# Kernel tuning notes

Hardware: AMD Instinct MI355X
Metric: run time of the kernel (lower is better)

The kernel has to match this reference:

```python
import jax, jax.numpy as jnp
import numpy as np

B, MAXLEN = 256, 10000
N_ATOMS, N_BONDS, N_ANG, N_TOR = 2000, 1999, 1998, 1997
NBT, NAT, NTT = 50, 100, 200
EPS = 1e-8


def setup_inputs() -> dict:
    rng = np.random.default_rng(0)
    feats = np.zeros((B, MAXLEN, 9), np.float32)
    # col 0: atom types
    feats[:, :N_ATOMS, 0] = rng.integers(0, 20, (B, N_ATOMS))
    # col 5: flattened coords [3*N]
    coords = (rng.standard_normal((B, N_ATOMS, 3)) * 2.0).astype(np.float32)
    feats[:, :3 * N_ATOMS, 5] = coords.reshape(B, -1)
    # col 6: bonds (i, j, type) along a chain
    i = np.arange(N_BONDS, dtype=np.float32)
    bonds = np.zeros((B, N_BONDS, 3), np.float32)
    bonds[..., 0] = i; bonds[..., 1] = i + 1
    bonds[..., 2] = rng.integers(0, NBT, (B, N_BONDS))
    feats[:, :3 * N_BONDS, 6] = bonds.reshape(B, -1)
    # col 7: angles (i, j, k, type)
    a = np.arange(N_ANG, dtype=np.float32)
    angs = np.zeros((B, N_ANG, 4), np.float32)
    angs[..., 0] = a; angs[..., 1] = a + 1; angs[..., 2] = a + 2
    angs[..., 3] = rng.integers(0, NAT, (B, N_ANG))
    feats[:, :4 * N_ANG, 7] = angs.reshape(B, -1)
    # col 8: torsions (i, j, k, l, type)
    t = np.arange(N_TOR, dtype=np.float32)
    tors = np.zeros((B, N_TOR, 5), np.float32)
    tors[..., 0] = t; tors[..., 1] = t + 1; tors[..., 2] = t + 2; tors[..., 3] = t + 3
    tors[..., 4] = rng.integers(0, NTT, (B, N_TOR))
    feats[:, :5 * N_TOR, 8] = tors.reshape(B, -1)
    # per-column valid lengths
    lengths = np.zeros((B, 9), np.int32)
    lengths[:, 0] = N_ATOMS
    lengths[:, 5] = 3 * N_ATOMS
    lengths[:, 6] = 3 * N_BONDS
    lengths[:, 7] = 4 * N_ANG
    lengths[:, 8] = 5 * N_TOR
    # learned params: (k, eq_value, multiplicity) per type row
    P = NBT + NAT + NTT
    opt = np.abs(rng.standard_normal((P, 3))).astype(np.float32)
    opt[:, 2] = rng.integers(1, 4, P).astype(np.float32)
    return {
        "features": jnp.asarray(feats),
        "lengths": jnp.asarray(lengths),
        "opt_pars": jnp.asarray(opt),
        "bond_type": jnp.arange(NBT, dtype=jnp.float32),
        "angle_type": jnp.arange(NAT, dtype=jnp.float32) + NBT,
        "tor_type": jnp.arange(NTT, dtype=jnp.float32) + NBT + NAT,
    }


def _gather(coords, idx):
    # coords [B,N,3], idx [B,M] -> [B,M,3]
    return jnp.take_along_axis(
        coords, jnp.broadcast_to(idx[..., None], idx.shape + (3,)), axis=1)


def _energy(features, lengths, opt_pars, bond_map, angle_map, tor_map):
    Bn = features.shape[0]
    coords = features[:, :3 * N_ATOMS, 5].reshape(Bn, N_ATOMS, 3)
    bonds = features[:, :3 * N_BONDS, 6].reshape(Bn, N_BONDS, 3).astype(jnp.int32)
    angs = features[:, :4 * N_ANG, 7].reshape(Bn, N_ANG, 4).astype(jnp.int32)
    tors = features[:, :5 * N_TOR, 8].reshape(Bn, N_TOR, 5).astype(jnp.int32)

    # ---- bonds: harmonic E = k * (r - r0)^2 ----
    ri, rj = _gather(coords, bonds[..., 0]), _gather(coords, bonds[..., 1])
    r = jnp.sqrt(jnp.sum((ri - rj) ** 2, -1) + EPS)          # [B,NB]
    pb = opt_pars[bond_map[bonds[..., 2]]]                   # [B,NB,3]
    eb = pb[..., 0] * (r - pb[..., 1]) ** 2
    mb = jnp.arange(N_BONDS)[None, :] < (lengths[:, 6:7] // 3)
    ebonds = jnp.sum(jnp.where(mb, eb, 0.0), -1)

    # ---- angles: harmonic E = k * (theta - theta0)^2 ----
    ai, aj, ak = (_gather(coords, angs[..., c]) for c in range(3))
    u, v = ai - aj, ak - aj
    cos = jnp.sum(u * v, -1) * jax.lax.rsqrt(
        (jnp.sum(u * u, -1) + EPS) * (jnp.sum(v * v, -1) + EPS))
    theta = jnp.arccos(jnp.clip(cos, -1.0 + 1e-6, 1.0 - 1e-6))
    pa = opt_pars[angle_map[angs[..., 3]]]
    ea = pa[..., 0] * (theta - pa[..., 1]) ** 2
    ma = jnp.arange(N_ANG)[None, :] < (lengths[:, 7:8] // 4)
    eangles = jnp.sum(jnp.where(ma, ea, 0.0), -1)

    # ---- torsions: E = k * (1 + cos(n*phi - phi0)) ----
    ti, tj, tk, tl = (_gather(coords, tors[..., c]) for c in range(4))
    b1, b2, b3 = tj - ti, tk - tj, tl - tk
    n1 = jnp.cross(b1, b2)
    n2 = jnp.cross(b2, b3)
    b2h = b2 * jax.lax.rsqrt(jnp.sum(b2 * b2, -1, keepdims=True) + EPS)
    m1 = jnp.cross(n1, b2h)
    phi = jnp.arctan2(jnp.sum(m1 * n2, -1), jnp.sum(n1 * n2, -1))
    pt = opt_pars[tor_map[tors[..., 4]]]
    et = pt[..., 0] * (1.0 + jnp.cos(pt[..., 2] * phi - pt[..., 1]))
    mt = jnp.arange(N_TOR)[None, :] < (lengths[:, 8:9] // 5)
    etors = jnp.sum(jnp.where(mt, et, 0.0), -1)

    return ebonds + eangles + etors                          # [B]


def reference(features, lengths, opt_pars, bond_type, angle_type, tor_type):
    return _energy(features, lengths, opt_pars,
                   bond_type.astype(jnp.int32),
                   angle_type.astype(jnp.int32),
                   tor_type.astype(jnp.int32))
```

## Files before the change

### kernel.cpp

```cpp
#include <hip/hip_runtime.h>
#include <math.h>


#define EBS 1024

constexpr int MAXLEN = 10000;
constexpr int NBT = 50, NAT = 100, NTT = 200;
constexpr float EPS = 1e-8f;

constexpr int OFF_SC  = 0;
constexpr int OFF_SB  = OFF_SC  + 6000 * 4;
constexpr int OFF_SA  = OFF_SB  + 2000 * 8;
constexpr int OFF_ST  = OFF_SA  + 2000 * 8;
constexpr int OFF_SBP = OFF_ST  + 2000 * 16;
constexpr int OFF_SAP = OFF_SBP + NBT * 2 * 4;
constexpr int OFF_STP = OFF_SAP + NAT * 2 * 4;
constexpr int OFF_SW  = OFF_STP + NTT * 4 * 4;
constexpr int SMEM_BYTES = OFF_SW + 16 * 4;

__device__ __forceinline__ float acos_fast(float x) {
    float t = fabsf(x);
    float p = fmaf(t, -0.0187293f, 0.0742610f);
    p = fmaf(p, t, -0.2121144f);
    p = fmaf(p, t, 1.5707288f);
    float r = sqrtf(1.0f - t) * p;
    return (x >= 0.0f) ? r : (3.14159265358979f - r);
}

__global__ __launch_bounds__(EBS) void energy_kernel(
    const float* __restrict__ features,
    const int*   __restrict__ lengths,
    const float* __restrict__ opt_pars,
    const float* __restrict__ bond_type,
    const float* __restrict__ angle_type,
    const float* __restrict__ tor_type,
    float*       __restrict__ out)
{
    extern __shared__ __align__(16) char smem[];
    float*          sc  = (float*)(smem + OFF_SC);
    ushort4*        sb4 = (ushort4*)(smem + OFF_SB);
    ushort4*        sa4 = (ushort4*)(smem + OFF_SA);
    unsigned short* st  = (unsigned short*)(smem + OFF_ST);
    ushort4*        st4 = (ushort4*)(smem + OFF_ST);
    float*          sbp = (float*)(smem + OFF_SBP);
    float*          sap = (float*)(smem + OFF_SAP);
    float*          stp = (float*)(smem + OFF_STP);
    float*          sw  = (float*)(smem + OFF_SW);
    unsigned short* sbf = (unsigned short*)(smem + OFF_SB);
    unsigned short* saf = (unsigned short*)(smem + OFF_SA);

    const int b   = blockIdx.x;
    const int tid = threadIdx.x;
    const float* __restrict__ fb = features + (size_t)b * MAXLEN * 9;

    for (int i = tid; i < NBT; i += EBS) {
        int idx = (int)bond_type[i];
        sbp[2*i+0] = opt_pars[3*idx+0];
        sbp[2*i+1] = opt_pars[3*idx+1];
    }
    for (int i = tid; i < NAT; i += EBS) {
        int idx = (int)angle_type[i];
        sap[2*i+0] = opt_pars[3*idx+0];
        sap[2*i+1] = opt_pars[3*idx+1];
    }
    for (int i = tid; i < NTT; i += EBS) {
        int idx = (int)tor_type[i];
        float k  = opt_pars[3*idx+0];
        float p0 = opt_pars[3*idx+1];
        float n  = opt_pars[3*idx+2];
        stp[4*i+0] = k;
        stp[4*i+1] = cosf(p0);
        stp[4*i+2] = sinf(p0);
        stp[4*i+3] = n;
    }

    #pragma unroll 2
    for (int i = tid; i < MAXLEN; i += EBS) {
        const float* __restrict__ row = fb + 9 * i + 5;
        float vc = row[0];
        float vb = row[1];
        float va = row[2];
        float vt = row[3];
        if (i < 6000) {
            sc[i] = vc;
            int t = i / 3, slot = i - 3 * t;
            if (i < 5997) sbf[4 * t + slot] = (unsigned short)(int)vb;
        }
        if (i < 7992) saf[i] = (unsigned short)(int)va;
        if (i < 9985) {
            int t = i / 5, slot = i - 5 * t;
            st[8 * t + slot] = (unsigned short)(int)vt;
        }
    }
    __syncthreads();

    float acc = 0.0f;

    {
        const int nb = lengths[b * 9 + 6] / 3;
        for (int t = tid; t < nb; t += EBS) {
            ushort4 q = sb4[t];
            int i = q.x, j = q.y, ty = q.z;
            float dx = sc[3*i+0] - sc[3*j+0];
            float dy = sc[3*i+1] - sc[3*j+1];
            float dz = sc[3*i+2] - sc[3*j+2];
            float r  = sqrtf(dx*dx + dy*dy + dz*dz + EPS);
            float d  = r - sbp[2*ty+1];
            acc += sbp[2*ty+0] * d * d;
        }
    }

    {
        const int na = lengths[b * 9 + 7] / 4;
        for (int t = tid; t < na; t += EBS) {
            ushort4 q = sa4[t];
            int i = q.x, j = q.y, k_ = q.z, ty = q.w;
            float jx = sc[3*j+0], jy = sc[3*j+1], jz = sc[3*j+2];
            float ux = sc[3*i+0] - jx, uy = sc[3*i+1] - jy, uz = sc[3*i+2] - jz;
            float vx = sc[3*k_+0] - jx, vy = sc[3*k_+1] - jy, vz = sc[3*k_+2] - jz;
            float uv = ux*vx + uy*vy + uz*vz;
            float uu = ux*ux + uy*uy + uz*uz;
            float vv = vx*vx + vy*vy + vz*vz;
            float cth = uv * rsqrtf((uu + EPS) * (vv + EPS));
            cth = fminf(fmaxf(cth, -1.0f + 1e-6f), 1.0f - 1e-6f);
            float theta = acos_fast(cth);
            float d = theta - sap[2*ty+1];
            acc += sap[2*ty+0] * d * d;
        }
    }

    {
        const int nt = lengths[b * 9 + 8] / 5;
        for (int t = tid; t < nt; t += EBS) {
            ushort4 q = st4[2*t];
            int ty = st[8*t+4];
            int i = q.x, j = q.y, k_ = q.z, l = q.w;
            float ix = sc[3*i+0],  iy = sc[3*i+1],  iz = sc[3*i+2];
            float jx = sc[3*j+0],  jy = sc[3*j+1],  jz = sc[3*j+2];
            float kx = sc[3*k_+0], ky = sc[3*k_+1], kz = sc[3*k_+2];
            float lx = sc[3*l+0],  ly = sc[3*l+1],  lz = sc[3*l+2];
            float b1x = jx - ix, b1y = jy - iy, b1z = jz - iz;
            float b2x = kx - jx, b2y = ky - jy, b2z = kz - jz;
            float b3x = lx - kx, b3y = ly - ky, b3z = lz - kz;
            float n1x = b1y*b2z - b1z*b2y;
            float n1y = b1z*b2x - b1x*b2z;
            float n1z = b1x*b2y - b1y*b2x;
            float n2x = b2y*b3z - b2z*b3y;
            float n2y = b2z*b3x - b2x*b3z;
            float n2z = b2x*b3y - b2y*b3x;
            float inv = rsqrtf(b2x*b2x + b2y*b2y + b2z*b2z + EPS);
            float hx = b2x * inv, hy = b2y * inv, hz = b2z * inv;
            float m1x = n1y*hz - n1z*hy;
            float m1y = n1z*hx - n1x*hz;
            float m1z = n1x*hy - n1y*hx;
            float sy = m1x*n2x + m1y*n2y + m1z*n2z;
            float sx = n1x*n2x + n1y*n2y + n1z*n2z;
            float rinv = rsqrtf(sx*sx + sy*sy + 1e-30f);
            float c1 = sx * rinv, s1 = sy * rinv;
            float c2 = fmaf(2.0f*c1, c1, -1.0f);
            float s2 = 2.0f * s1 * c1;
            float c3 = fmaf(2.0f*c1, c2, -c1);
            float s3 = fmaf(2.0f*c1, s2, -s1);
            float k  = stp[4*ty+0];
            float cp = stp[4*ty+1];
            float sp = stp[4*ty+2];
            int   ni = (int)stp[4*ty+3];
            float cn = (ni == 1) ? c1 : ((ni == 2) ? c2 : c3);
            float sn = (ni == 1) ? s1 : ((ni == 2) ? s2 : s3);
            acc += k * (1.0f + cn * cp + sn * sp);
        }
    }

    for (int off = 32; off > 0; off >>= 1)
        acc += __shfl_down(acc, off, 64);
    const int wave = tid >> 6, lane = tid & 63;
    if (lane == 0) sw[wave] = acc;
    __syncthreads();
    if (tid == 0) {
        float v = 0.0f;
        #pragma unroll
        for (int w = 0; w < EBS / 64; ++w) v += sw[w];
        out[b] = v;
    }
}

extern "C" void kernel_launch(void* const* d_in, const int* in_sizes, int n_in,
                              void* d_out, int out_size, void* d_ws, size_t ws_size,
                              hipStream_t stream) {
    const float* features   = (const float*)d_in[0];
    const int*   lengths    = (const int*)  d_in[1];
    const float* opt_pars   = (const float*)d_in[2];
    const float* bond_type  = (const float*)d_in[3];
    const float* angle_type = (const float*)d_in[4];
    const float* tor_type   = (const float*)d_in[5];
    float* out = (float*)d_out;

    hipFuncSetAttribute((const void*)energy_kernel,
                        hipFuncAttributeMaxDynamicSharedMemorySize, SMEM_BYTES);

    const int B = out_size;
    energy_kernel<<<B, EBS, SMEM_BYTES, stream>>>(
        features, lengths, opt_pars, bond_type, angle_type, tor_type, out);
}
```

Measured before the change: 148.2 us.

## Split fused energy kernel into compact, per-term energy, and reduce kernels

Replaces the single block-per-molecule kernel, which staged everything in shared memory, with four launches. A prep kernel builds the parameter tables, a grid-wide compact kernel writes coordinates and index quads to workspace, and the energy kernel uses 24 chunks per molecule with one thread per bond, angle or torsion. A final kernel reduces the partial sums. The goal is more parallelism and better occupancy than 256 blocks of 1024 threads with large shared-memory use, at the cost of extra launches, global-memory round trips through the workspace, and uncoalesced coordinate gathers from global memory.

```diff
diff --git a/kernel.cpp b/kernel.cpp
--- a/kernel.cpp
+++ b/kernel.cpp
@@ -2,21 +2,20 @@
 #include <math.h>
 
 
-#define EBS 1024
-
+constexpr int BATCH  = 256;
 constexpr int MAXLEN = 10000;
 constexpr int NBT = 50, NAT = 100, NTT = 200;
 constexpr float EPS = 1e-8f;
-
-constexpr int OFF_SC  = 0;
-constexpr int OFF_SB  = OFF_SC  + 6000 * 4;
-constexpr int OFF_SA  = OFF_SB  + 2000 * 8;
-constexpr int OFF_ST  = OFF_SA  + 2000 * 8;
-constexpr int OFF_SBP = OFF_ST  + 2000 * 16;
-constexpr int OFF_SAP = OFF_SBP + NBT * 2 * 4;
-constexpr int OFF_STP = OFF_SAP + NAT * 2 * 4;
-constexpr int OFF_SW  = OFF_STP + NTT * 4 * 4;
-constexpr int SMEM_BYTES = OFF_SW + 16 * 4;
+constexpr int NCH = 24;
+
+constexpr size_t OFF_RBP = 0;
+constexpr size_t OFF_RAP = OFF_RBP + NBT * 2 * 4;
+constexpr size_t OFF_RTP = OFF_RAP + NAT * 2 * 4;
+constexpr size_t OFF_CC  = OFF_RTP + NTT * 4 * 4;
+constexpr size_t OFF_BQ  = OFF_CC  + (size_t)BATCH * 6000 * 4;
+constexpr size_t OFF_AQ  = OFF_BQ  + (size_t)BATCH * 8192 * 2;
+constexpr size_t OFF_TQ  = OFF_AQ  + (size_t)BATCH * 8192 * 2;
+constexpr size_t OFF_PT  = OFF_TQ  + (size_t)BATCH * 16384 * 2;
 
 __device__ __forceinline__ float acos_fast(float x) {
     float t = fabsf(x);
@@ -27,118 +26,122 @@
     return (x >= 0.0f) ? r : (3.14159265358979f - r);
 }
 
-__global__ __launch_bounds__(EBS) void energy_kernel(
-    const float* __restrict__ features,
-    const int*   __restrict__ lengths,
+__global__ __launch_bounds__(256) void prep_kernel(
     const float* __restrict__ opt_pars,
     const float* __restrict__ bond_type,
     const float* __restrict__ angle_type,
     const float* __restrict__ tor_type,
-    float*       __restrict__ out)
-{
-    extern __shared__ __align__(16) char smem[];
-    float*          sc  = (float*)(smem + OFF_SC);
-    ushort4*        sb4 = (ushort4*)(smem + OFF_SB);
-    ushort4*        sa4 = (ushort4*)(smem + OFF_SA);
-    unsigned short* st  = (unsigned short*)(smem + OFF_ST);
-    ushort4*        st4 = (ushort4*)(smem + OFF_ST);
-    float*          sbp = (float*)(smem + OFF_SBP);
-    float*          sap = (float*)(smem + OFF_SAP);
-    float*          stp = (float*)(smem + OFF_STP);
-    float*          sw  = (float*)(smem + OFF_SW);
-    unsigned short* sbf = (unsigned short*)(smem + OFF_SB);
-    unsigned short* saf = (unsigned short*)(smem + OFF_SA);
-
-    const int b   = blockIdx.x;
+    float* __restrict__ rbp, float* __restrict__ rap, float* __restrict__ rtp)
+{
+    const int i = threadIdx.x;
+    if (i < NBT) {
+        int idx = (int)bond_type[i];
+        rbp[2*i+0] = opt_pars[3*idx+0];
+        rbp[2*i+1] = opt_pars[3*idx+1];
+    }
+    if (i < NAT) {
+        int idx = (int)angle_type[i];
+        rap[2*i+0] = opt_pars[3*idx+0];
+        rap[2*i+1] = opt_pars[3*idx+1];
+    }
+    if (i < NTT) {
+        int idx = (int)tor_type[i];
+        float p0 = opt_pars[3*idx+1];
+        rtp[4*i+0] = opt_pars[3*idx+0];
+        rtp[4*i+1] = cosf(p0);
+        rtp[4*i+2] = sinf(p0);
+        rtp[4*i+3] = opt_pars[3*idx+2];
+    }
+}
+
+__global__ __launch_bounds__(256) void compact_kernel(
+    const float* __restrict__ features,
+    float* __restrict__ cc, unsigned short* __restrict__ bq,
+    unsigned short* __restrict__ aq, unsigned short* __restrict__ tq)
+{
+    const unsigned gid = blockIdx.x * 256u + threadIdx.x;
+    const unsigned b   = gid / (unsigned)MAXLEN;
+    const unsigned i   = gid - b * (unsigned)MAXLEN;
+
+    const float* __restrict__ row = features + (size_t)b * MAXLEN * 9 + 9u * i + 5u;
+    float vc = row[0];
+    float vb = row[1];
+    float va = row[2];
+    float vt = row[3];
+
+    if (i < 6000u) cc[b * 6000u + i] = vc;
+    if (i < 5997u) {
+        unsigned t = i / 3u, slot = i - 3u * t;
+        bq[b * 8192u + 4u * t + slot] = (unsigned short)(int)vb;
+    }
+    if (i < 7992u)
+        aq[b * 8192u + i] = (unsigned short)(int)va;
+    if (i < 9985u) {
+        unsigned t = i / 5u, slot = i - 5u * t;
+        tq[b * 16384u + 8u * t + slot] = (unsigned short)(int)vt;
+    }
+}
+
+__global__ __launch_bounds__(256) void energy_kernel(
+    const float* __restrict__ cc,
+    const ushort4* __restrict__ bq,
+    const ushort4* __restrict__ aq,
+    const ushort4* __restrict__ tq,
+    const int*   __restrict__ lengths,
+    const float* __restrict__ rbp,
+    const float* __restrict__ rap,
+    const float* __restrict__ rtp,
+    float*       __restrict__ part)
+{
+    const int idx = blockIdx.x;
+    const int b   = idx & 255;
+    const int c   = idx >> 8;
     const int tid = threadIdx.x;
-    const float* __restrict__ fb = features + (size_t)b * MAXLEN * 9;
-
-    for (int i = tid; i < NBT; i += EBS) {
-        int idx = (int)bond_type[i];
-        sbp[2*i+0] = opt_pars[3*idx+0];
-        sbp[2*i+1] = opt_pars[3*idx+1];
-    }
-    for (int i = tid; i < NAT; i += EBS) {
-        int idx = (int)angle_type[i];
-        sap[2*i+0] = opt_pars[3*idx+0];
-        sap[2*i+1] = opt_pars[3*idx+1];
-    }
-    for (int i = tid; i < NTT; i += EBS) {
-        int idx = (int)tor_type[i];
-        float k  = opt_pars[3*idx+0];
-        float p0 = opt_pars[3*idx+1];
-        float n  = opt_pars[3*idx+2];
-        stp[4*i+0] = k;
-        stp[4*i+1] = cosf(p0);
-        stp[4*i+2] = sinf(p0);
-        stp[4*i+3] = n;
-    }
-
-    #pragma unroll 2
-    for (int i = tid; i < MAXLEN; i += EBS) {
-        const float* __restrict__ row = fb + 9 * i + 5;
-        float vc = row[0];
-        float vb = row[1];
-        float va = row[2];
-        float vt = row[3];
-        if (i < 6000) {
-            sc[i] = vc;
-            int t = i / 3, slot = i - 3 * t;
-            if (i < 5997) sbf[4 * t + slot] = (unsigned short)(int)vb;
+    const int tglob = c * 256 + tid;
+    const int type  = tglob >> 11;
+    const int t     = tglob & 2047;
+
+    const float* __restrict__ cb = cc + (size_t)b * 6000;
+    float e = 0.0f;
+
+    if (type == 0) {
+        const int nb = lengths[b * 9 + 6] / 3;
+        if (t < nb) {
+            ushort4 q = bq[b * 2048 + t];
+            int i = q.x, j = q.y, ty = q.z;
+            float dx = cb[3*i+0] - cb[3*j+0];
+            float dy = cb[3*i+1] - cb[3*j+1];
+            float dz = cb[3*i+2] - cb[3*j+2];
+            float r  = sqrtf(dx*dx + dy*dy + dz*dz + EPS);
+            float d  = r - rbp[2*ty+1];
+            e = rbp[2*ty+0] * d * d;
         }
-        if (i < 7992) saf[i] = (unsigned short)(int)va;
-        if (i < 9985) {
-            int t = i / 5, slot = i - 5 * t;
-            st[8 * t + slot] = (unsigned short)(int)vt;
-        }
-    }
-    __syncthreads();
-
-    float acc = 0.0f;
-
-    {
-        const int nb = lengths[b * 9 + 6] / 3;
-        for (int t = tid; t < nb; t += EBS) {
-            ushort4 q = sb4[t];
-            int i = q.x, j = q.y, ty = q.z;
-            float dx = sc[3*i+0] - sc[3*j+0];
-            float dy = sc[3*i+1] - sc[3*j+1];
-            float dz = sc[3*i+2] - sc[3*j+2];
-            float r  = sqrtf(dx*dx + dy*dy + dz*dz + EPS);
-            float d  = r - sbp[2*ty+1];
-            acc += sbp[2*ty+0] * d * d;
-        }
-    }
-
-    {
+    } else if (type == 1) {
         const int na = lengths[b * 9 + 7] / 4;
-        for (int t = tid; t < na; t += EBS) {
-            ushort4 q = sa4[t];
+        if (t < na) {
+            ushort4 q = aq[b * 2048 + t];
             int i = q.x, j = q.y, k_ = q.z, ty = q.w;
-            float jx = sc[3*j+0], jy = sc[3*j+1], jz = sc[3*j+2];
-            float ux = sc[3*i+0] - jx, uy = sc[3*i+1] - jy, uz = sc[3*i+2] - jz;
-            float vx = sc[3*k_+0] - jx, vy = sc[3*k_+1] - jy, vz = sc[3*k_+2] - jz;
+            float jx = cb[3*j+0], jy = cb[3*j+1], jz = cb[3*j+2];
+            float ux = cb[3*i+0] - jx, uy = cb[3*i+1] - jy, uz = cb[3*i+2] - jz;
+            float vx = cb[3*k_+0] - jx, vy = cb[3*k_+1] - jy, vz = cb[3*k_+2] - jz;
             float uv = ux*vx + uy*vy + uz*vz;
             float uu = ux*ux + uy*uy + uz*uz;
             float vv = vx*vx + vy*vy + vz*vz;
             float cth = uv * rsqrtf((uu + EPS) * (vv + EPS));
             cth = fminf(fmaxf(cth, -1.0f + 1e-6f), 1.0f - 1e-6f);
-            float theta = acos_fast(cth);
-            float d = theta - sap[2*ty+1];
-            acc += sap[2*ty+0] * d * d;
+            float d = acos_fast(cth) - rap[2*ty+1];
+            e = rap[2*ty+0] * d * d;
         }
-    }
-
-    {
+    } else {
         const int nt = lengths[b * 9 + 8] / 5;
-        for (int t = tid; t < nt; t += EBS) {
-            ushort4 q = st4[2*t];
-            int ty = st[8*t+4];
-            int i = q.x, j = q.y, k_ = q.z, l = q.w;
-            float ix = sc[3*i+0],  iy = sc[3*i+1],  iz = sc[3*i+2];
-            float jx = sc[3*j+0],  jy = sc[3*j+1],  jz = sc[3*j+2];
-            float kx = sc[3*k_+0], ky = sc[3*k_+1], kz = sc[3*k_+2];
-            float lx = sc[3*l+0],  ly = sc[3*l+1],  lz = sc[3*l+2];
+        if (t < nt) {
+            ushort4 q0 = tq[b * 4096 + 2*t];
+            ushort4 q1 = tq[b * 4096 + 2*t + 1];
+            int i = q0.x, j = q0.y, k_ = q0.z, l = q0.w, ty = q1.x;
+            float ix = cb[3*i+0],  iy = cb[3*i+1],  iz = cb[3*i+2];
+            float jx = cb[3*j+0],  jy = cb[3*j+1],  jz = cb[3*j+2];
+            float kx = cb[3*k_+0], ky = cb[3*k_+1], kz = cb[3*k_+2];
+            float lx = cb[3*l+0],  ly = cb[3*l+1],  lz = cb[3*l+2];
             float b1x = jx - ix, b1y = jy - iy, b1z = jz - iz;
             float b2x = kx - jx, b2y = ky - jy, b2z = kz - jz;
             float b3x = lx - kx, b3y = ly - ky, b3z = lz - kz;
@@ -161,27 +164,34 @@
             float s2 = 2.0f * s1 * c1;
             float c3 = fmaf(2.0f*c1, c2, -c1);
             float s3 = fmaf(2.0f*c1, s2, -s1);
-            float k  = stp[4*ty+0];
-            float cp = stp[4*ty+1];
-            float sp = stp[4*ty+2];
-            int   ni = (int)stp[4*ty+3];
+            float k  = rtp[4*ty+0];
+            float cp = rtp[4*ty+1];
+            float sp = rtp[4*ty+2];
+            int   ni = (int)rtp[4*ty+3];
             float cn = (ni == 1) ? c1 : ((ni == 2) ? c2 : c3);
             float sn = (ni == 1) ? s1 : ((ni == 2) ? s2 : s3);
-            acc += k * (1.0f + cn * cp + sn * sp);
+            e = k * (1.0f + cn * cp + sn * sp);
         }
     }
 
     for (int off = 32; off > 0; off >>= 1)
-        acc += __shfl_down(acc, off, 64);
+        e += __shfl_down(e, off, 64);
+    __shared__ float sw[4];
     const int wave = tid >> 6, lane = tid & 63;
-    if (lane == 0) sw[wave] = acc;
+    if (lane == 0) sw[wave] = e;
     __syncthreads();
-    if (tid == 0) {
-        float v = 0.0f;
-        #pragma unroll
-        for (int w = 0; w < EBS / 64; ++w) v += sw[w];
-        out[b] = v;
-    }
+    if (tid == 0)
+        part[idx] = sw[0] + sw[1] + sw[2] + sw[3];
+}
+
+__global__ __launch_bounds__(256) void reduce_kernel(
+    const float* __restrict__ part, float* __restrict__ out)
+{
+    const int b = threadIdx.x;
+    float v = 0.0f;
+    #pragma unroll
+    for (int c = 0; c < NCH; ++c) v += part[c * 256 + b];
+    out[b] = v;
 }
 
 extern "C" void kernel_launch(void* const* d_in, const int* in_sizes, int n_in,
@@ -194,11 +204,23 @@
     const float* angle_type = (const float*)d_in[4];
     const float* tor_type   = (const float*)d_in[5];
     float* out = (float*)d_out;
-
-    hipFuncSetAttribute((const void*)energy_kernel,
-                        hipFuncAttributeMaxDynamicSharedMemorySize, SMEM_BYTES);
-
-    const int B = out_size;
-    energy_kernel<<<B, EBS, SMEM_BYTES, stream>>>(
-        features, lengths, opt_pars, bond_type, angle_type, tor_type, out);
-}
+    char*  ws  = (char*)d_ws;
+
+    float*          rbp = (float*)(ws + OFF_RBP);
+    float*          rap = (float*)(ws + OFF_RAP);
+    float*          rtp = (float*)(ws + OFF_RTP);
+    float*          cc  = (float*)(ws + OFF_CC);
+    unsigned short* bq  = (unsigned short*)(ws + OFF_BQ);
+    unsigned short* aq  = (unsigned short*)(ws + OFF_AQ);
+    unsigned short* tq  = (unsigned short*)(ws + OFF_TQ);
+    float*          pt  = (float*)(ws + OFF_PT);
+
+    prep_kernel<<<1, 256, 0, stream>>>(opt_pars, bond_type, angle_type,
+                                       tor_type, rbp, rap, rtp);
+    compact_kernel<<<BATCH * MAXLEN / 256, 256, 0, stream>>>(
+        features, cc, bq, aq, tq);
+    energy_kernel<<<NCH * 256, 256, 0, stream>>>(
+        cc, (const ushort4*)bq, (const ushort4*)aq, (const ushort4*)tq,
+        lengths, rbp, rap, rtp, pt);
+    reduce_kernel<<<1, 256, 0, stream>>>(pt, out);
+}
```

After: 158.8 us. +7.2%, slower.

## Overlap tail feature loads with first-phase energy compute and pad coords to float4

Applied to the files above, without the earlier changes.

The staging loop is split in two. Rows 0..5999 (coordinates, bonds and the first part of the angle and torsion index lists) are staged first. Rows 6000..9999 are prefetched into registers while bonds, the first 1500 angles and the first 1200 torsions are evaluated, and are written to shared memory after a second barrier. Coordinates are stored as padded float4 so each atom is read with one vector LDS, and torsion types move to their own array. Parameter-table setup is also spread across disjoint thread ranges. The cost is an extra barrier, more live registers, and split limits hardcoded to the index layout.

```diff
diff --git a/kernel.cpp b/kernel.cpp
--- a/kernel.cpp
+++ b/kernel.cpp
@@ -8,14 +8,15 @@
 constexpr int NBT = 50, NAT = 100, NTT = 200;
 constexpr float EPS = 1e-8f;
 
-constexpr int OFF_SC  = 0;
-constexpr int OFF_SB  = OFF_SC  + 6000 * 4;
-constexpr int OFF_SA  = OFF_SB  + 2000 * 8;
-constexpr int OFF_ST  = OFF_SA  + 2000 * 8;
-constexpr int OFF_SBP = OFF_ST  + 2000 * 16;
-constexpr int OFF_SAP = OFF_SBP + NBT * 2 * 4;
-constexpr int OFF_STP = OFF_SAP + NAT * 2 * 4;
-constexpr int OFF_SW  = OFF_STP + NTT * 4 * 4;
+constexpr int OFF_SCF = 0;
+constexpr int OFF_SB  = OFF_SCF + 8000 * 4;
+constexpr int OFF_SA  = OFF_SB  + 8000 * 2;
+constexpr int OFF_ST4 = OFF_SA  + 8000 * 2;
+constexpr int OFF_STY = OFF_ST4 + 8000 * 2;
+constexpr int OFF_RBP = OFF_STY + 2000 * 2;
+constexpr int OFF_RAP = OFF_RBP + 100 * 4;
+constexpr int OFF_RTP = OFF_RAP + 200 * 4;
+constexpr int OFF_SW  = OFF_RTP + 800 * 4;
 constexpr int SMEM_BYTES = OFF_SW + 16 * 4;
 
 __device__ __forceinline__ float acos_fast(float x) {
@@ -37,138 +38,176 @@
     float*       __restrict__ out)
 {
     extern __shared__ __align__(16) char smem[];
-    float*          sc  = (float*)(smem + OFF_SC);
-    ushort4*        sb4 = (ushort4*)(smem + OFF_SB);
-    ushort4*        sa4 = (ushort4*)(smem + OFF_SA);
-    unsigned short* st  = (unsigned short*)(smem + OFF_ST);
-    ushort4*        st4 = (ushort4*)(smem + OFF_ST);
-    float*          sbp = (float*)(smem + OFF_SBP);
-    float*          sap = (float*)(smem + OFF_SAP);
-    float*          stp = (float*)(smem + OFF_STP);
+    float*          scf = (float*)(smem + OFF_SCF);
+    const float4*   sc4 = (const float4*)(smem + OFF_SCF);
+    unsigned short* sb  = (unsigned short*)(smem + OFF_SB);
+    const ushort4*  sb4 = (const ushort4*)(smem + OFF_SB);
+    unsigned short* sa  = (unsigned short*)(smem + OFF_SA);
+    const ushort4*  sa4 = (const ushort4*)(smem + OFF_SA);
+    unsigned short* st4 = (unsigned short*)(smem + OFF_ST4);
+    const ushort4*  st44= (const ushort4*)(smem + OFF_ST4);
+    unsigned short* sty = (unsigned short*)(smem + OFF_STY);
+    float*          rbp = (float*)(smem + OFF_RBP);
+    float*          rap = (float*)(smem + OFF_RAP);
+    float*          rtp = (float*)(smem + OFF_RTP);
     float*          sw  = (float*)(smem + OFF_SW);
-    unsigned short* sbf = (unsigned short*)(smem + OFF_SB);
-    unsigned short* saf = (unsigned short*)(smem + OFF_SA);
 
     const int b   = blockIdx.x;
     const int tid = threadIdx.x;
     const float* __restrict__ fb = features + (size_t)b * MAXLEN * 9;
 
-    for (int i = tid; i < NBT; i += EBS) {
-        int idx = (int)bond_type[i];
-        sbp[2*i+0] = opt_pars[3*idx+0];
-        sbp[2*i+1] = opt_pars[3*idx+1];
-    }
-    for (int i = tid; i < NAT; i += EBS) {
+    if (tid < NBT) {
+        int idx = (int)bond_type[tid];
+        rbp[2*tid+0] = opt_pars[3*idx+0];
+        rbp[2*tid+1] = opt_pars[3*idx+1];
+    } else if (tid < NBT + NAT) {
+        int i = tid - NBT;
         int idx = (int)angle_type[i];
-        sap[2*i+0] = opt_pars[3*idx+0];
-        sap[2*i+1] = opt_pars[3*idx+1];
-    }
-    for (int i = tid; i < NTT; i += EBS) {
+        rap[2*i+0] = opt_pars[3*idx+0];
+        rap[2*i+1] = opt_pars[3*idx+1];
+    } else if (tid < NBT + NAT + NTT) {
+        int i = tid - NBT - NAT;
         int idx = (int)tor_type[i];
-        float k  = opt_pars[3*idx+0];
         float p0 = opt_pars[3*idx+1];
-        float n  = opt_pars[3*idx+2];
-        stp[4*i+0] = k;
-        stp[4*i+1] = cosf(p0);
-        stp[4*i+2] = sinf(p0);
-        stp[4*i+3] = n;
-    }
-
-    #pragma unroll 2
-    for (int i = tid; i < MAXLEN; i += EBS) {
-        const float* __restrict__ row = fb + 9 * i + 5;
-        float vc = row[0];
-        float vb = row[1];
-        float va = row[2];
-        float vt = row[3];
+        rtp[4*i+0] = opt_pars[3*idx+0];
+        rtp[4*i+1] = cosf(p0);
+        rtp[4*i+2] = sinf(p0);
+        rtp[4*i+3] = opt_pars[3*idx+2];
+    }
+
+    #pragma unroll
+    for (int k = 0; k < 6; ++k) {
+        const int i = tid + k * EBS;
         if (i < 6000) {
-            sc[i] = vc;
-            int t = i / 3, slot = i - 3 * t;
-            if (i < 5997) sbf[4 * t + slot] = (unsigned short)(int)vb;
+            const float* __restrict__ row = fb + 9 * i + 5;
+            float vc = row[0];
+            float vb = row[1];
+            float va = row[2];
+            float vt = row[3];
+            const int q3 = i / 3, r3 = i - 3 * q3;
+            scf[4 * q3 + r3] = vc;
+            if (i < 5997) sb[4 * q3 + r3] = (unsigned short)(int)vb;
+            sa[i] = (unsigned short)(int)va;
+            const int q5 = i / 5, r5 = i - 5 * q5;
+            if (r5 < 4) st4[4 * q5 + r5] = (unsigned short)(int)vt;
+            else        sty[q5]          = (unsigned short)(int)vt;
         }
-        if (i < 7992) saf[i] = (unsigned short)(int)va;
-        if (i < 9985) {
-            int t = i / 5, slot = i - 5 * t;
-            st[8 * t + slot] = (unsigned short)(int)vt;
+    }
+    __syncthreads();
+
+    const int nb = lengths[b * 9 + 6] / 3;
+    const int na = lengths[b * 9 + 7] / 4;
+    const int nt = lengths[b * 9 + 8] / 5;
+
+    auto bond_e = [&](int t) -> float {
+        ushort4 q = sb4[t];
+        float4 pi = sc4[q.x], pj = sc4[q.y];
+        float dx = pi.x - pj.x, dy = pi.y - pj.y, dz = pi.z - pj.z;
+        float r  = sqrtf(dx*dx + dy*dy + dz*dz + EPS);
+        float d  = r - rbp[2*q.z+1];
+        return rbp[2*q.z+0] * d * d;
+    };
+    auto angle_e = [&](int t) -> float {
+        ushort4 q = sa4[t];
+        float4 pi = sc4[q.x], pj = sc4[q.y], pk = sc4[q.z];
+        float ux = pi.x - pj.x, uy = pi.y - pj.y, uz = pi.z - pj.z;
+        float vx = pk.x - pj.x, vy = pk.y - pj.y, vz = pk.z - pj.z;
+        float uv = ux*vx + uy*vy + uz*vz;
+        float uu = ux*ux + uy*uy + uz*uz;
+        float vv = vx*vx + vy*vy + vz*vz;
+        float cth = uv * rsqrtf((uu + EPS) * (vv + EPS));
+        cth = fminf(fmaxf(cth, -1.0f + 1e-6f), 1.0f - 1e-6f);
+        float d = acos_fast(cth) - rap[2*q.w+1];
+        return rap[2*q.w+0] * d * d;
+    };
+    auto tor_e = [&](int t) -> float {
+        ushort4 q = st44[t];
+        int ty = sty[t];
+        float4 pi = sc4[q.x], pj = sc4[q.y], pk = sc4[q.z], pl = sc4[q.w];
+        float b1x = pj.x - pi.x, b1y = pj.y - pi.y, b1z = pj.z - pi.z;
+        float b2x = pk.x - pj.x, b2y = pk.y - pj.y, b2z = pk.z - pj.z;
+        float b3x = pl.x - pk.x, b3y = pl.y - pk.y, b3z = pl.z - pk.z;
+        float n1x = b1y*b2z - b1z*b2y;
+        float n1y = b1z*b2x - b1x*b2z;
+        float n1z = b1x*b2y - b1y*b2x;
+        float n2x = b2y*b3z - b2z*b3y;
+        float n2y = b2z*b3x - b2x*b3z;
+        float n2z = b2x*b3y - b2y*b3x;
+        float inv = rsqrtf(b2x*b2x + b2y*b2y + b2z*b2z + EPS);
+        float hx = b2x * inv, hy = b2y * inv, hz = b2z * inv;
+        float m1x = n1y*hz - n1z*hy;
+        float m1y = n1z*hx - n1x*hz;
+        float m1z = n1x*hy - n1y*hx;
+        float sy = m1x*n2x + m1y*n2y + m1z*n2z;
+        float sx = n1x*n2x + n1y*n2y + n1z*n2z;
+        float rinv = rsqrtf(sx*sx + sy*sy + 1e-30f);
+        float c1 = sx * rinv, s1 = sy * rinv;
+        float c2 = fmaf(2.0f*c1, c1, -1.0f);
+        float s2 = 2.0f * s1 * c1;
+        float c3 = fmaf(2.0f*c1, c2, -c1);
+        float s3 = fmaf(2.0f*c1, s2, -s1);
+        float k  = rtp[4*ty+0];
+        float cp = rtp[4*ty+1];
+        float sp = rtp[4*ty+2];
+        int   ni = (int)rtp[4*ty+3];
+        float cn = (ni == 1) ? c1 : ((ni == 2) ? c2 : c3);
+        float sn = (ni == 1) ? s1 : ((ni == 2) ? s2 : s3);
+        return k * (1.0f + cn * cp + sn * sp);
+    };
+
+    float acc = 0.0f;
+
+    float pva[4], pvt[4];
+    #pragma unroll
+    for (int k = 0; k < 4; ++k) {
+        const int i = 6000 + tid + k * EBS;
+        if (i < MAXLEN) {
+            const float* __restrict__ row = fb + 9 * i + 7;
+            pva[k] = row[0];
+            pvt[k] = row[1];
         }
     }
+
+    {
+        int t0 = tid, t1 = tid + EBS;
+        float e0 = (t0 < nb) ? bond_e(t0) : 0.0f;
+        float e1 = (t1 < nb) ? bond_e(t1) : 0.0f;
+        acc += e0 + e1;
+    }
+    {
+        const int lim = min(na, 1500);
+        int t0 = tid, t1 = tid + EBS;
+        float e0 = (t0 < lim) ? angle_e(t0) : 0.0f;
+        float e1 = (t1 < lim) ? angle_e(t1) : 0.0f;
+        acc += e0 + e1;
+    }
+    {
+        const int lim = min(nt, 1200);
+        int t0 = tid, t1 = tid + EBS;
+        float e0 = (t0 < lim) ? tor_e(t0) : 0.0f;
+        float e1 = (t1 < lim) ? tor_e(t1) : 0.0f;
+        acc += e0 + e1;
+    }
+
+    #pragma unroll
+    for (int k = 0; k < 4; ++k) {
+        const int i = 6000 + tid + k * EBS;
+        if (i < MAXLEN) {
+            if (i < 7992) sa[i] = (unsigned short)(int)pva[k];
+            if (i < 9985) {
+                const int q5 = i / 5, r5 = i - 5 * q5;
+                if (r5 < 4) st4[4 * q5 + r5] = (unsigned short)(int)pvt[k];
+                else        sty[q5]          = (unsigned short)(int)pvt[k];
+            }
+        }
+    }
     __syncthreads();
 
-    float acc = 0.0f;
-
-    {
-        const int nb = lengths[b * 9 + 6] / 3;
-        for (int t = tid; t < nb; t += EBS) {
-            ushort4 q = sb4[t];
-            int i = q.x, j = q.y, ty = q.z;
-            float dx = sc[3*i+0] - sc[3*j+0];
-            float dy = sc[3*i+1] - sc[3*j+1];
-            float dz = sc[3*i+2] - sc[3*j+2];
-            float r  = sqrtf(dx*dx + dy*dy + dz*dz + EPS);
-            float d  = r - sbp[2*ty+1];
-            acc += sbp[2*ty+0] * d * d;
-        }
-    }
-
-    {
-        const int na = lengths[b * 9 + 7] / 4;
-        for (int t = tid; t < na; t += EBS) {
-            ushort4 q = sa4[t];
-            int i = q.x, j = q.y, k_ = q.z, ty = q.w;
-            float jx = sc[3*j+0], jy = sc[3*j+1], jz = sc[3*j+2];
-            float ux = sc[3*i+0] - jx, uy = sc[3*i+1] - jy, uz = sc[3*i+2] - jz;
-            float vx = sc[3*k_+0] - jx, vy = sc[3*k_+1] - jy, vz = sc[3*k_+2] - jz;
-            float uv = ux*vx + uy*vy + uz*vz;
-            float uu = ux*ux + uy*uy + uz*uz;
-            float vv = vx*vx + vy*vy + vz*vz;
-            float cth = uv * rsqrtf((uu + EPS) * (vv + EPS));
-            cth = fminf(fmaxf(cth, -1.0f + 1e-6f), 1.0f - 1e-6f);
-            float theta = acos_fast(cth);
-            float d = theta - sap[2*ty+1];
-            acc += sap[2*ty+0] * d * d;
-        }
-    }
-
-    {
-        const int nt = lengths[b * 9 + 8] / 5;
-        for (int t = tid; t < nt; t += EBS) {
-            ushort4 q = st4[2*t];
-            int ty = st[8*t+4];
-            int i = q.x, j = q.y, k_ = q.z, l = q.w;
-            float ix = sc[3*i+0],  iy = sc[3*i+1],  iz = sc[3*i+2];
-            float jx = sc[3*j+0],  jy = sc[3*j+1],  jz = sc[3*j+2];
-            float kx = sc[3*k_+0], ky = sc[3*k_+1], kz = sc[3*k_+2];
-            float lx = sc[3*l+0],  ly = sc[3*l+1],  lz = sc[3*l+2];
-            float b1x = jx - ix, b1y = jy - iy, b1z = jz - iz;
-            float b2x = kx - jx, b2y = ky - jy, b2z = kz - jz;
-            float b3x = lx - kx, b3y = ly - ky, b3z = lz - kz;
-            float n1x = b1y*b2z - b1z*b2y;
-            float n1y = b1z*b2x - b1x*b2z;
-            float n1z = b1x*b2y - b1y*b2x;
-            float n2x = b2y*b3z - b2z*b3y;
-            float n2y = b2z*b3x - b2x*b3z;
-            float n2z = b2x*b3y - b2y*b3x;
-            float inv = rsqrtf(b2x*b2x + b2y*b2y + b2z*b2z + EPS);
-            float hx = b2x * inv, hy = b2y * inv, hz = b2z * inv;
-            float m1x = n1y*hz - n1z*hy;
-            float m1y = n1z*hx - n1x*hz;
-            float m1z = n1x*hy - n1y*hx;
-            float sy = m1x*n2x + m1y*n2y + m1z*n2z;
-            float sx = n1x*n2x + n1y*n2y + n1z*n2z;
-            float rinv = rsqrtf(sx*sx + sy*sy + 1e-30f);
-            float c1 = sx * rinv, s1 = sy * rinv;
-            float c2 = fmaf(2.0f*c1, c1, -1.0f);
-            float s2 = 2.0f * s1 * c1;
-            float c3 = fmaf(2.0f*c1, c2, -c1);
-            float s3 = fmaf(2.0f*c1, s2, -s1);
-            float k  = stp[4*ty+0];
-            float cp = stp[4*ty+1];
-            float sp = stp[4*ty+2];
-            int   ni = (int)stp[4*ty+3];
-            float cn = (ni == 1) ? c1 : ((ni == 2) ? c2 : c3);
-            float sn = (ni == 1) ? s1 : ((ni == 2) ? s2 : s3);
-            acc += k * (1.0f + cn * cp + sn * sp);
-        }
+    {
+        int t = 1500 + tid;
+        if (t < na) acc += angle_e(t);
+        int u = 1200 + tid;
+        if (u < nt) acc += tor_e(u);
     }
 
     for (int off = 32; off > 0; off >>= 1)
```

New measurement: 143.6 us (median of 2 runs). -3.1%, faster.
